# Kernel optimization log

Hardware: AMD Instinct MI355X
Metric: run time of the kernel (lower is better)

Reference implementation:

```python
import jax, jax.numpy as jnp
import numpy as np

N_NODES = 100000
N_EDGES = 400000
D = 128           # vector_dim
N_GRAPHS = 4096
N_LAYERS = 5
IN_FEAT = 11


def setup_inputs() -> dict:
    key = jax.random.key(0)
    ks = jax.random.split(key, 6)
    x = jax.random.uniform(ks[0], (N_NODES, IN_FEAT), dtype=jnp.float32)
    edge_index = jax.random.randint(ks[1], (2, N_EDGES), 0, N_NODES, dtype=jnp.int64)
    batch = jnp.sort(jax.random.randint(ks[2], (N_NODES,), 0, N_GRAPHS, dtype=jnp.int64))
    # expansion Linear(11, D)
    We = jax.random.normal(ks[3], (IN_FEAT, D), dtype=jnp.float32) * (1.0 / np.sqrt(IN_FEAT))
    be = jnp.zeros((D,), dtype=jnp.float32)
    # stacked GCNConv weights/biases for 5 layers
    Wg = jax.random.normal(ks[4], (N_LAYERS, D, D), dtype=jnp.float32) * (1.0 / np.sqrt(D))
    bg = jnp.zeros((N_LAYERS, D), dtype=jnp.float32)
    return {"x": x, "edge_index": edge_index, "batch": batch, "num_graphs": N_GRAPHS,
            "We": We, "be": be, "Wg": Wg, "bg": bg}


def reference(x, edge_index, batch, num_graphs, We, be, Wg, bg):
    n = x.shape[0]
    src, dst = edge_index[0], edge_index[1]
    # GCNConv(improved=True): self-loop weight 2 -> deg[i] = in_degree + 2
    deg = jax.ops.segment_sum(jnp.ones((src.shape[0],), x.dtype), dst, num_segments=n) + 2.0
    dinv = deg ** -0.5
    enorm = dinv[src] * dinv[dst]          # per-edge symmetric norm [E]
    self_norm = 2.0 * dinv * dinv          # self-loop contribution [N]

    h = jnp.log(x + 1.0) @ We + be         # expansion [N, D]
    for l in range(Wg.shape[0]):
        t = h @ Wg[l]                      # [N, D]
        agg = jax.ops.segment_sum(t[src] * enorm[:, None], dst, num_segments=n)
        agg = agg + self_norm[:, None] * t + bg[l]
        h = h + jax.nn.relu(agg)           # residual; dropout = identity (eval)
    return jax.ops.segment_sum(h, batch, num_segments=num_graphs)  # global_add_pool [G, D]
```

## Files before the change

### kernel.cpp

```cpp
#include <hip/hip_runtime.h>
#include <hip/hip_bf16.h>

#define NN 100000
#define NE 400000
#define DD 128
#define NG 4096
#define NL 5
#define NF 11
#define GROWS 100096

typedef __attribute__((ext_vector_type(8))) __bf16 bf16x8;
typedef __attribute__((ext_vector_type(4))) float f32x4;


__global__ void deg_kernel(const int* __restrict__ ei, int* __restrict__ deg) {
    int e = blockIdx.x * 256 + threadIdx.x;
    if (e < NE) atomicAdd(&deg[ei[NE + e]], 1);
}

__global__ void scan1_kernel(const int* __restrict__ deg, int* __restrict__ off,
                             int* __restrict__ bsums) {
    __shared__ int lds[256];
    int tid = threadIdx.x, b = blockIdx.x;
    int base = b * 1024 + tid * 4;
    int v[4];
#pragma unroll
    for (int q = 0; q < 4; ++q) {
        int i = base + q;
        v[q] = (i < NN) ? deg[i] : 0;
    }
    int s = v[0] + v[1] + v[2] + v[3];
    lds[tid] = s;
    __syncthreads();
    for (int o = 1; o < 256; o <<= 1) {
        int t2 = (tid >= o) ? lds[tid - o] : 0;
        __syncthreads();
        lds[tid] += t2;
        __syncthreads();
    }
    int p = lds[tid] - s;
#pragma unroll
    for (int q = 0; q < 4; ++q) {
        int i = base + q;
        if (i < NN) off[i] = p;
        p += v[q];
    }
    if (tid == 255) bsums[b] = lds[255];
}

__global__ void scan2_kernel(int* __restrict__ bsums, int nb) {
    __shared__ int lds[128];
    int tid = threadIdx.x;
    int v = (tid < nb) ? bsums[tid] : 0;
    lds[tid] = v;
    __syncthreads();
    for (int o = 1; o < 128; o <<= 1) {
        int t2 = (tid >= o) ? lds[tid - o] : 0;
        __syncthreads();
        lds[tid] += t2;
        __syncthreads();
    }
    if (tid < nb) bsums[tid] = lds[tid] - v;
}

__global__ void finish_kernel(int* __restrict__ off, const int* __restrict__ bsums,
                              const int* __restrict__ deg, float* __restrict__ dinv) {
    int i = blockIdx.x * 256 + threadIdx.x;
    if (i == 0) off[NN] = NE;
    if (i < NN) {
        off[i] += bsums[i >> 10];
        dinv[i] = rsqrtf((float)deg[i] + 2.0f);
    }
}

__global__ void fill_kernel(const int* __restrict__ ei, const int* __restrict__ off,
                            int* __restrict__ cursor, int2* __restrict__ csr,
                            const float* __restrict__ dinv) {
    int e = blockIdx.x * 256 + threadIdx.x;
    if (e >= NE) return;
    int s = ei[e];
    int d = ei[NE + e];
    int pos = off[d] + atomicAdd(&cursor[d], 1);
    csr[pos] = make_int2(s, __float_as_int(dinv[s] * dinv[d]));
}


__global__ void wpack_kernel(const float* __restrict__ Wg, unsigned short* __restrict__ whi,
                             unsigned short* __restrict__ wlo) {
    int t = blockIdx.x * 256 + threadIdx.x;
    int l = t >> 14, r = t & 16383;
    int k = r >> 7, n = r & 127;
    float w = Wg[(size_t)l * 16384 + k * 128 + n];
    __bf16 hb = (__bf16)w;
    float lo = w - (float)hb;
    __bf16 lb = (__bf16)lo;
    int ft = n >> 4, kc = k >> 5, lane = (((k >> 3) & 3) << 4) | (n & 15), i = k & 7;
    size_t idx = (size_t)l * 16384 + (((ft * 4 + kc) * 64 + lane) * 8 + i);
    whi[idx] = __builtin_bit_cast(unsigned short, hb);
    wlo[idx] = __builtin_bit_cast(unsigned short, lb);
}


__global__ __launch_bounds__(256) void expand_kernel(const float* __restrict__ x,
                                                     const float* __restrict__ We,
                                                     const float* __restrict__ be,
                                                     float* __restrict__ h) {
    __shared__ float ls[2 * NF];
    const int tid = threadIdx.x;
    const int node0 = blockIdx.x * 2;
    if (tid < 2 * NF) ls[tid] = __logf(x[(size_t)node0 * NF + tid] + 1.0f);
    __syncthreads();
    const int row = tid >> 7, j = tid & 127;
    float acc = be[j];
#pragma unroll
    for (int f = 0; f < NF; ++f) {
        acc = fmaf(ls[row * NF + f], We[f * DD + j], acc);
    }
    h[(size_t)(node0 + row) * DD + j] = acc;
}


__global__ __launch_bounds__(256) void agg_kernel(const float* __restrict__ h,
                                                  float* __restrict__ g,
                                                  const int* __restrict__ off,
                                                  const int2* __restrict__ csr,
                                                  const float* __restrict__ dinv) {
    const int tid = threadIdx.x;
    const int node = blockIdx.x * 8 + (tid >> 5);
    const int jj = tid & 31;
    const float4* __restrict__ h4 = (const float4*)h;

    float di = dinv[node];
    float sn = 2.0f * di * di;
    float4 hv = h4[(size_t)node * 32 + jj];
    float4 acc = make_float4(sn * hv.x, sn * hv.y, sn * hv.z, sn * hv.w);

    const int e0 = off[node];
    const int e1 = off[node + 1];
#pragma unroll 1
    for (int e = e0; e < e1; e += 4) {
        const int eL = e1 - 1;
        int2 r0 = csr[e];
        int2 r1 = csr[min(e + 1, eL)];
        int2 r2 = csr[min(e + 2, eL)];
        int2 r3 = csr[min(e + 3, eL)];
        float4 v0 = h4[(size_t)r0.x * 32 + jj];
        float4 v1 = h4[(size_t)r1.x * 32 + jj];
        float4 v2 = h4[(size_t)r2.x * 32 + jj];
        float4 v3 = h4[(size_t)r3.x * 32 + jj];
        float w0 = __int_as_float(r0.y);
        float w1 = (e + 1 < e1) ? __int_as_float(r1.y) : 0.f;
        float w2 = (e + 2 < e1) ? __int_as_float(r2.y) : 0.f;
        float w3 = (e + 3 < e1) ? __int_as_float(r3.y) : 0.f;
        acc.x = fmaf(w0, v0.x, acc.x); acc.y = fmaf(w0, v0.y, acc.y);
        acc.z = fmaf(w0, v0.z, acc.z); acc.w = fmaf(w0, v0.w, acc.w);
        acc.x = fmaf(w1, v1.x, acc.x); acc.y = fmaf(w1, v1.y, acc.y);
        acc.z = fmaf(w1, v1.z, acc.z); acc.w = fmaf(w1, v1.w, acc.w);
        acc.x = fmaf(w2, v2.x, acc.x); acc.y = fmaf(w2, v2.y, acc.y);
        acc.z = fmaf(w2, v2.z, acc.z); acc.w = fmaf(w2, v2.w, acc.w);
        acc.x = fmaf(w3, v3.x, acc.x); acc.y = fmaf(w3, v3.y, acc.y);
        acc.z = fmaf(w3, v3.z, acc.z); acc.w = fmaf(w3, v3.w, acc.w);
    }
    ((float4*)g)[(size_t)node * 32 + jj] = acc;
}


__global__ __launch_bounds__(256) void mfma_gemm(const float* __restrict__ g,
                                                 float* __restrict__ h,
                                                 const unsigned short* __restrict__ whi,
                                                 const unsigned short* __restrict__ wlo,
                                                 const float* __restrict__ b) {
    const int lane = threadIdx.x & 63;
    const int wv = threadIdx.x >> 6;
    const int nbase = blockIdx.x * 128 + wv * 32 + (lane & 15);
    const int kg = lane >> 4;

    bf16x8 gh[2][4], gl[2][4];
#pragma unroll
    for (int nt = 0; nt < 2; ++nt) {
        const float* gp = g + (size_t)(nbase + nt * 16) * DD + kg * 8;
#pragma unroll
        for (int kc = 0; kc < 4; ++kc) {
            float4 f0 = *(const float4*)(gp + kc * 32);
            float4 f1 = *(const float4*)(gp + kc * 32 + 4);
            float t[8] = {f0.x, f0.y, f0.z, f0.w, f1.x, f1.y, f1.z, f1.w};
#pragma unroll
            for (int i = 0; i < 8; ++i) {
                __bf16 hi = (__bf16)t[i];
                float lo = t[i] - (float)hi;
                gh[nt][kc][i] = hi;
                gl[nt][kc][i] = (__bf16)lo;
            }
        }
    }

    f32x4 c[2][8];
#pragma unroll
    for (int nt = 0; nt < 2; ++nt)
#pragma unroll
        for (int ft = 0; ft < 8; ++ft) c[nt][ft] = (f32x4){0.f, 0.f, 0.f, 0.f};

#pragma unroll
    for (int kc = 0; kc < 4; ++kc) {
#pragma unroll
        for (int ft = 0; ft < 8; ++ft) {
            size_t boff = (size_t)(((ft * 4 + kc) * 64 + lane) * 8);
            bf16x8 wh = *(const bf16x8*)(whi + boff);
            bf16x8 wl = *(const bf16x8*)(wlo + boff);
#pragma unroll
            for (int nt = 0; nt < 2; ++nt) {
                c[nt][ft] = __builtin_amdgcn_mfma_f32_16x16x32_bf16(wh, gh[nt][kc], c[nt][ft], 0, 0, 0);
                c[nt][ft] = __builtin_amdgcn_mfma_f32_16x16x32_bf16(wl, gh[nt][kc], c[nt][ft], 0, 0, 0);
                c[nt][ft] = __builtin_amdgcn_mfma_f32_16x16x32_bf16(wh, gl[nt][kc], c[nt][ft], 0, 0, 0);
            }
        }
    }

    const int f0 = kg * 4;
#pragma unroll
    for (int nt = 0; nt < 2; ++nt) {
        const int node = nbase + nt * 16;
        if (node < NN) {
#pragma unroll
            for (int ft = 0; ft < 8; ++ft) {
                size_t o = (size_t)node * DD + ft * 16 + f0;
                float4 hv = *(const float4*)(h + o);
                float4 bv = *(const float4*)(b + ft * 16 + f0);
                hv.x += fmaxf(c[nt][ft][0] + bv.x, 0.f);
                hv.y += fmaxf(c[nt][ft][1] + bv.y, 0.f);
                hv.z += fmaxf(c[nt][ft][2] + bv.z, 0.f);
                hv.w += fmaxf(c[nt][ft][3] + bv.w, 0.f);
                *(float4*)(h + o) = hv;
            }
        }
    }
}


__global__ void pool_kernel(const float* __restrict__ h, const int* __restrict__ batch,
                            float* __restrict__ out) {
    int j = threadIdx.x;
    int n0 = blockIdx.x * 64;
    float acc = 0.f;
    int prev = -1;
    for (int n = 0; n < 64; ++n) {
        int i = n0 + n;
        if (i >= NN) break;
        int bi = batch[i];
        if (bi != prev) {
            if (prev >= 0) atomicAdd(&out[(size_t)prev * DD + j], acc);
            acc = 0.f;
            prev = bi;
        }
        acc += h[(size_t)i * DD + j];
    }
    if (prev >= 0) atomicAdd(&out[(size_t)prev * DD + j], acc);
}


static inline size_t align_up(size_t x, size_t a) { return (x + a - 1) & ~(a - 1); }

extern "C" void kernel_launch(void* const* d_in, const int* in_sizes, int n_in,
                              void* d_out, int out_size, void* d_ws, size_t ws_size,
                              hipStream_t stream) {
    const float* x   = (const float*)d_in[0];
    const int*   ei  = (const int*)d_in[1];
    const int*   bat = (const int*)d_in[2];
    const float* We  = (const float*)d_in[4];
    const float* be  = (const float*)d_in[5];
    const float* Wg  = (const float*)d_in[6];
    const float* bg  = (const float*)d_in[7];
    float* out = (float*)d_out;

    char* p = (char*)d_ws;
    size_t o = 0;
    float* h = (float*)(p + o);       o = align_up(o + (size_t)NN * DD * 4, 512);
    float* g = (float*)(p + o);       o = align_up(o + (size_t)GROWS * DD * 4, 512);
    float* dinv = (float*)(p + o);    o = align_up(o + (size_t)NN * 4, 512);
    int* deg = (int*)(p + o);         o = align_up(o + (size_t)NN * 4, 512);
    int* cursor = (int*)(p + o);      o = align_up(o + (size_t)NN * 4, 512);
    int* off = (int*)(p + o);         o = align_up(o + (size_t)(NN + 1) * 4, 512);
    int* bsums = (int*)(p + o);       o = align_up(o + 512, 512);
    int2* csr = (int2*)(p + o);       o = align_up(o + (size_t)NE * 8, 512);
    unsigned short* whi = (unsigned short*)(p + o); o = align_up(o + (size_t)NL * 16384 * 2, 512);
    unsigned short* wlo = (unsigned short*)(p + o); o = align_up(o + (size_t)NL * 16384 * 2, 512);
    (void)ws_size; (void)in_sizes; (void)n_in; (void)out_size;

    const int GRID_E = (NE + 255) / 256;
    const int GRID_SCAN1 = (NN + 1023) / 1024;
    const int GRID_N256 = (NN + 255) / 256;
    const int GRID_EXP = NN / 2;
    const int GRID_AGG = NN / 8;
    const int GRID_GEMM = GROWS / 128;
    const int GRID_POOL = (NN + 63) / 64;
    const int GRID_WPACK = NL * 16384 / 256;

    hipMemsetAsync(deg, 0, (size_t)NN * 4, stream);
    hipMemsetAsync(cursor, 0, (size_t)NN * 4, stream);
    hipMemsetAsync(out, 0, (size_t)NG * DD * 4, stream);

    deg_kernel<<<GRID_E, 256, 0, stream>>>(ei, deg);
    scan1_kernel<<<GRID_SCAN1, 256, 0, stream>>>(deg, off, bsums);
    scan2_kernel<<<1, 128, 0, stream>>>(bsums, GRID_SCAN1);
    finish_kernel<<<GRID_N256, 256, 0, stream>>>(off, bsums, deg, dinv);
    fill_kernel<<<GRID_E, 256, 0, stream>>>(ei, off, cursor, csr, dinv);
    wpack_kernel<<<GRID_WPACK, 256, 0, stream>>>(Wg, whi, wlo);

    expand_kernel<<<GRID_EXP, 256, 0, stream>>>(x, We, be, h);

    for (int l = 0; l < NL; ++l) {
        agg_kernel<<<GRID_AGG, 256, 0, stream>>>(h, g, off, csr, dinv);
        mfma_gemm<<<GRID_GEMM, 256, 0, stream>>>(g, h,
                                                 whi + (size_t)l * 16384,
                                                 wlo + (size_t)l * 16384,
                                                 bg + (size_t)l * DD);
    }

    pool_kernel<<<GRID_POOL, 128, 0, stream>>>(h, bat, out);
}
```

Baseline: 603.0 us.

## Emit pre-split bf16 hi/lo operands in MFMA fragment layout from aggregation

The aggregation kernel now performs the fp32-to-bf16 hi/lo split itself and writes both halves directly in the MFMA operand fragment layout. The GEMM then loads ready-made bf16x8 fragments instead of reading fp32 rows and converting them. The GEMM is also reorganized to one 16-node tile per wave with half the nodes per block and twice the blocks. Intermediate traffic stays the same in bytes, but the conversion moves out of the GEMM and its loads become contiguous. The cost is less weight-fragment reuse per wave in the GEMM and scattered 8-byte stores from the aggregation kernel.

After: 601.9 us. Within noise of the previous version (-0.2%).

```diff
diff --git a/kernel.cpp b/kernel.cpp
--- a/kernel.cpp
+++ b/kernel.cpp
@@ -121,7 +121,8 @@
 
 
 __global__ __launch_bounds__(256) void agg_kernel(const float* __restrict__ h,
-                                                  float* __restrict__ g,
+                                                  unsigned short* __restrict__ gbh,
+                                                  unsigned short* __restrict__ gbl,
                                                   const int* __restrict__ off,
                                                   const int2* __restrict__ csr,
                                                   const float* __restrict__ dinv) {
@@ -161,44 +162,51 @@
         acc.x = fmaf(w3, v3.x, acc.x); acc.y = fmaf(w3, v3.y, acc.y);
         acc.z = fmaf(w3, v3.z, acc.z); acc.w = fmaf(w3, v3.w, acc.w);
     }
-    ((float4*)g)[(size_t)node * 32 + jj] = acc;
-}
-
-
-__global__ __launch_bounds__(256) void mfma_gemm(const float* __restrict__ g,
+
+    __bf16 h0 = (__bf16)acc.x; __bf16 l0 = (__bf16)(acc.x - (float)h0);
+    __bf16 h1 = (__bf16)acc.y; __bf16 l1 = (__bf16)(acc.y - (float)h1);
+    __bf16 h2 = (__bf16)acc.z; __bf16 l2 = (__bf16)(acc.z - (float)h2);
+    __bf16 h3 = (__bf16)acc.w; __bf16 l3 = (__bf16)(acc.w - (float)h3);
+    const int tile = node >> 4;
+    const int kc = jj >> 3;
+    const int kg = (jj >> 1) & 3;
+    const int i0 = (jj & 1) * 4;
+    const int lanep = (kg << 4) | (node & 15);
+    size_t base = (((size_t)tile * 4 + kc) * 64 + lanep) * 8 + i0;
+    ushort4 hs = make_ushort4(__builtin_bit_cast(unsigned short, h0),
+                              __builtin_bit_cast(unsigned short, h1),
+                              __builtin_bit_cast(unsigned short, h2),
+                              __builtin_bit_cast(unsigned short, h3));
+    ushort4 ls = make_ushort4(__builtin_bit_cast(unsigned short, l0),
+                              __builtin_bit_cast(unsigned short, l1),
+                              __builtin_bit_cast(unsigned short, l2),
+                              __builtin_bit_cast(unsigned short, l3));
+    *(ushort4*)(gbh + base) = hs;
+    *(ushort4*)(gbl + base) = ls;
+}
+
+
+__global__ __launch_bounds__(256) void mfma_gemm(const unsigned short* __restrict__ gbh,
+                                                 const unsigned short* __restrict__ gbl,
                                                  float* __restrict__ h,
                                                  const unsigned short* __restrict__ whi,
                                                  const unsigned short* __restrict__ wlo,
                                                  const float* __restrict__ b) {
     const int lane = threadIdx.x & 63;
     const int wv = threadIdx.x >> 6;
-    const int nbase = blockIdx.x * 128 + wv * 32 + (lane & 15);
-    const int kg = lane >> 4;
-
-    bf16x8 gh[2][4], gl[2][4];
-#pragma unroll
-    for (int nt = 0; nt < 2; ++nt) {
-        const float* gp = g + (size_t)(nbase + nt * 16) * DD + kg * 8;
-#pragma unroll
-        for (int kc = 0; kc < 4; ++kc) {
-            float4 f0 = *(const float4*)(gp + kc * 32);
-            float4 f1 = *(const float4*)(gp + kc * 32 + 4);
-            float t[8] = {f0.x, f0.y, f0.z, f0.w, f1.x, f1.y, f1.z, f1.w};
-#pragma unroll
-            for (int i = 0; i < 8; ++i) {
-                __bf16 hi = (__bf16)t[i];
-                float lo = t[i] - (float)hi;
-                gh[nt][kc][i] = hi;
-                gl[nt][kc][i] = (__bf16)lo;
-            }
-        }
-    }
-
-    f32x4 c[2][8];
-#pragma unroll
-    for (int nt = 0; nt < 2; ++nt)
-#pragma unroll
-        for (int ft = 0; ft < 8; ++ft) c[nt][ft] = (f32x4){0.f, 0.f, 0.f, 0.f};
+    const int nbase = blockIdx.x * 64 + wv * 16;
+    const size_t tbase = ((size_t)(nbase >> 4) * 4 * 64 + lane) * 8;
+
+    bf16x8 gh[4], gl[4];
+#pragma unroll
+    for (int kc = 0; kc < 4; ++kc) {
+        gh[kc] = *(const bf16x8*)(gbh + tbase + kc * 512);
+        gl[kc] = *(const bf16x8*)(gbl + tbase + kc * 512);
+    }
+
+    f32x4 c[8];
+#pragma unroll
+    for (int ft = 0; ft < 8; ++ft) c[ft] = (f32x4){0.f, 0.f, 0.f, 0.f};
 
 #pragma unroll
     for (int kc = 0; kc < 4; ++kc) {
@@ -207,31 +215,25 @@
             size_t boff = (size_t)(((ft * 4 + kc) * 64 + lane) * 8);
             bf16x8 wh = *(const bf16x8*)(whi + boff);
             bf16x8 wl = *(const bf16x8*)(wlo + boff);
-#pragma unroll
-            for (int nt = 0; nt < 2; ++nt) {
-                c[nt][ft] = __builtin_amdgcn_mfma_f32_16x16x32_bf16(wh, gh[nt][kc], c[nt][ft], 0, 0, 0);
-                c[nt][ft] = __builtin_amdgcn_mfma_f32_16x16x32_bf16(wl, gh[nt][kc], c[nt][ft], 0, 0, 0);
-                c[nt][ft] = __builtin_amdgcn_mfma_f32_16x16x32_bf16(wh, gl[nt][kc], c[nt][ft], 0, 0, 0);
-            }
+            c[ft] = __builtin_amdgcn_mfma_f32_16x16x32_bf16(wh, gh[kc], c[ft], 0, 0, 0);
+            c[ft] = __builtin_amdgcn_mfma_f32_16x16x32_bf16(wl, gh[kc], c[ft], 0, 0, 0);
+            c[ft] = __builtin_amdgcn_mfma_f32_16x16x32_bf16(wh, gl[kc], c[ft], 0, 0, 0);
         }
     }
 
-    const int f0 = kg * 4;
-#pragma unroll
-    for (int nt = 0; nt < 2; ++nt) {
-        const int node = nbase + nt * 16;
-        if (node < NN) {
-#pragma unroll
-            for (int ft = 0; ft < 8; ++ft) {
-                size_t o = (size_t)node * DD + ft * 16 + f0;
-                float4 hv = *(const float4*)(h + o);
-                float4 bv = *(const float4*)(b + ft * 16 + f0);
-                hv.x += fmaxf(c[nt][ft][0] + bv.x, 0.f);
-                hv.y += fmaxf(c[nt][ft][1] + bv.y, 0.f);
-                hv.z += fmaxf(c[nt][ft][2] + bv.z, 0.f);
-                hv.w += fmaxf(c[nt][ft][3] + bv.w, 0.f);
-                *(float4*)(h + o) = hv;
-            }
+    const int node = nbase + (lane & 15);
+    const int f0 = (lane >> 4) * 4;
+    if (node < NN) {
+#pragma unroll
+        for (int ft = 0; ft < 8; ++ft) {
+            size_t o = (size_t)node * DD + ft * 16 + f0;
+            float4 hv = *(const float4*)(h + o);
+            float4 bv = *(const float4*)(b + ft * 16 + f0);
+            hv.x += fmaxf(c[ft][0] + bv.x, 0.f);
+            hv.y += fmaxf(c[ft][1] + bv.y, 0.f);
+            hv.z += fmaxf(c[ft][2] + bv.z, 0.f);
+            hv.w += fmaxf(c[ft][3] + bv.w, 0.f);
+            *(float4*)(h + o) = hv;
         }
     }
 }
@@ -275,7 +277,8 @@
     char* p = (char*)d_ws;
     size_t o = 0;
     float* h = (float*)(p + o);       o = align_up(o + (size_t)NN * DD * 4, 512);
-    float* g = (float*)(p + o);       o = align_up(o + (size_t)GROWS * DD * 4, 512);
+    unsigned short* gbh = (unsigned short*)(p + o); o = align_up(o + (size_t)GROWS * DD * 2, 512);
+    unsigned short* gbl = (unsigned short*)(p + o); o = align_up(o + (size_t)GROWS * DD * 2, 512);
     float* dinv = (float*)(p + o);    o = align_up(o + (size_t)NN * 4, 512);
     int* deg = (int*)(p + o);         o = align_up(o + (size_t)NN * 4, 512);
     int* cursor = (int*)(p + o);      o = align_up(o + (size_t)NN * 4, 512);
@@ -291,7 +294,7 @@
     const int GRID_N256 = (NN + 255) / 256;
     const int GRID_EXP = NN / 2;
     const int GRID_AGG = NN / 8;
-    const int GRID_GEMM = GROWS / 128;
+    const int GRID_GEMM = GROWS / 64;
     const int GRID_POOL = (NN + 63) / 64;
     const int GRID_WPACK = NL * 16384 / 256;
 
@@ -309,8 +312,8 @@
     expand_kernel<<<GRID_EXP, 256, 0, stream>>>(x, We, be, h);
 
     for (int l = 0; l < NL; ++l) {
-        agg_kernel<<<GRID_AGG, 256, 0, stream>>>(h, g, off, csr, dinv);
-        mfma_gemm<<<GRID_GEMM, 256, 0, stream>>>(g, h,
+        agg_kernel<<<GRID_AGG, 256, 0, stream>>>(h, gbh, gbl, off, csr, dinv);
+        mfma_gemm<<<GRID_GEMM, 256, 0, stream>>>(gbh, gbl, h,
                                                  whi + (size_t)l * 16384,
                                                  wlo + (size_t)l * 16384,
                                                  bg + (size_t)l * DD);
```
